# Performance work log

Hardware: AMD Instinct MI355X
Metric: run time of the kernel (lower is better)

## Reference

```python
import jax, jax.numpy as jnp
import numpy as np

N_EXPERTS = 8
TOP_K = 2
HIDDEN = 768
INTER = 2048

def setup_inputs() -> dict:
    key = jax.random.key(0)
    ks = jax.random.split(key, 12)
    s_in = 1.0 / np.sqrt(HIDDEN)
    s_mid = 1.0 / np.sqrt(INTER)
    return {
        "x": jax.random.normal(ks[0], (4, 64, 64, HIDDEN), dtype=jnp.float32),
        # gate: nn.Parameter(randn(E, d))
        "gate_w": jax.random.normal(ks[1], (N_EXPERTS, HIDDEN), dtype=jnp.float32),
        # routed experts, stacked: fc1 (d->f), fc2 (f->d)
        "fc1_w": jax.random.uniform(ks[2], (N_EXPERTS, INTER, HIDDEN), jnp.float32, -s_in, s_in),
        "fc1_b": jax.random.uniform(ks[3], (N_EXPERTS, INTER), jnp.float32, -s_in, s_in),
        "fc2_w": jax.random.uniform(ks[4], (N_EXPERTS, HIDDEN, INTER), jnp.float32, -s_mid, s_mid),
        "fc2_b": jax.random.uniform(ks[5], (N_EXPERTS, HIDDEN), jnp.float32, -s_mid, s_mid),
        # shared MLP (gated): w1 (d->f), w3 (d->f), w2 (f->d)
        "w1_w": jax.random.uniform(ks[6], (INTER, HIDDEN), jnp.float32, -s_in, s_in),
        "w1_b": jax.random.uniform(ks[7], (INTER,), jnp.float32, -s_in, s_in),
        "w3_w": jax.random.uniform(ks[8], (INTER, HIDDEN), jnp.float32, -s_in, s_in),
        "w3_b": jax.random.uniform(ks[9], (INTER,), jnp.float32, -s_in, s_in),
        "w2_w": jax.random.uniform(ks[10], (HIDDEN, INTER), jnp.float32, -s_mid, s_mid),
        "w2_b": jax.random.uniform(ks[11], (HIDDEN,), jnp.float32, -s_mid, s_mid),
    }

def _gelu(h):
    # torch nn.GELU / F.gelu default = exact (erf) form
    return jax.nn.gelu(h, approximate=False)

def reference(x, gate_w, fc1_w, fc1_b, fc2_w, fc2_b,
              w1_w, w1_b, w3_w, w3_b, w2_w, w2_b):
    B, H, W, C = x.shape
    xf = x.reshape(-1, C)                                  # [T, d]
    # gate: softmax over experts, top-k, renormalize
    scores = jax.nn.softmax(xf @ gate_w.T, axis=-1)        # [T, E]
    top_v, top_i = jax.lax.top_k(scores, TOP_K)            # [T, k]
    top_v = top_v / jnp.sum(top_v, axis=-1, keepdims=True)
    # routed experts: dense-mask combine (weight 0 => zero contribution,
    # same math as gather-GEMM-scatter without data-dependent shapes)
    out = jnp.zeros_like(xf)
    for e in range(N_EXPERTS):
        w_e = jnp.sum(jnp.where(top_i == e, top_v, 0.0), axis=-1)   # [T]
        h = _gelu(xf @ fc1_w[e].T + fc1_b[e])                        # [T, f]
        y = h @ fc2_w[e].T + fc2_b[e]                                # [T, d]
        out = out + w_e[:, None] * y
    # shared gated MLP
    shared = (_gelu(xf @ w1_w.T + w1_b) * (xf @ w3_w.T + w3_b)) @ w2_w.T + w2_b
    return (out + shared).reshape(B, H, W, C)
```

## Files before the change

### kernel.cpp

```cpp
#include <hip/hip_runtime.h>
#include <math.h>

#define T_TOK 16384
#define DH 768
#define DF 2048
#define NE 8
#define NSLOT (2 * T_TOK)
#define MT_ROUTED 264
#define NROW_H (MT_ROUTED * 128)

typedef __attribute__((ext_vector_type(8))) short bf16x8;
typedef __attribute__((ext_vector_type(4))) float f32x4;

__device__ __forceinline__ unsigned short f2bf(float f) {
  union { float f; unsigned int u; } v; v.f = f;
  unsigned int u = v.u;
  u += 0x7fffu + ((u >> 16) & 1u);
  return (unsigned short)(u >> 16);
}
__device__ __forceinline__ float bf2f(unsigned short s) {
  union { unsigned int u; float f; } v; v.u = ((unsigned int)s) << 16; return v.f;
}

__device__ __forceinline__ float gelu_exact(float x) {
  return 0.5f * x * (1.0f + erff(x * 0.70710678118654752440f));
}

__device__ __forceinline__ unsigned short* yrow(unsigned short* ylo,
                                                unsigned short* yhi, int s) {
  return (s < T_TOK) ? (ylo + (long)s * DH) : (yhi + (long)(s - T_TOK) * DH);
}

__device__ __forceinline__ void async_cp16(void* lds, const void* g) {
  __builtin_amdgcn_global_load_lds(
      (const __attribute__((address_space(1))) unsigned int*)(unsigned long long)g,
      (__attribute__((address_space(3))) unsigned int*)(unsigned int)(unsigned long long)lds,
      16, 0, 0);
}

__global__ __launch_bounds__(256) void conv_f32_bf16(
    const float* __restrict__ src, unsigned short* __restrict__ dst, int n4) {
  int i = blockIdx.x * blockDim.x + threadIdx.x;
  if (i >= n4) return;
  const float4 v = ((const float4*)src)[i];
  union { unsigned short us[4]; unsigned long long u64; } o;
  o.us[0] = f2bf(v.x); o.us[1] = f2bf(v.y); o.us[2] = f2bf(v.z); o.us[3] = f2bf(v.w);
  ((unsigned long long*)dst)[i] = o.u64;
}

__global__ __launch_bounds__(256) void gate_topk(
    const float* __restrict__ x, const float* __restrict__ gw,
    unsigned short* __restrict__ xb, int* __restrict__ eids,
    float* __restrict__ wts) {
  const int wave = threadIdx.x >> 6;
  const int lane = threadIdx.x & 63;
  const int t = blockIdx.x * 4 + wave;
  float4 xv[3];
#pragma unroll
  for (int i = 0; i < 3; ++i) {
    const int c = i * 256 + lane * 4;
    xv[i] = *(const float4*)&x[(long)t * DH + c];
    ushort4 o;
    o.x = f2bf(xv[i].x); o.y = f2bf(xv[i].y);
    o.z = f2bf(xv[i].z); o.w = f2bf(xv[i].w);
    *(ushort4*)&xb[(long)t * DH + c] = o;
  }
  float s[NE];
#pragma unroll
  for (int e = 0; e < NE; ++e) {
    float a = 0.f;
#pragma unroll
    for (int i = 0; i < 3; ++i) {
      const float4 g = *(const float4*)&gw[e * DH + i * 256 + lane * 4];
      a += xv[i].x * g.x + xv[i].y * g.y + xv[i].z * g.z + xv[i].w * g.w;
    }
    s[e] = a;
  }
#pragma unroll
  for (int off = 32; off >= 1; off >>= 1) {
#pragma unroll
    for (int e = 0; e < NE; ++e) s[e] += __shfl_xor(s[e], off);
  }
  if (lane == 0) {
    float b1 = s[0]; int i1 = 0;
#pragma unroll
    for (int e = 1; e < NE; ++e) { if (s[e] > b1) { b1 = s[e]; i1 = e; } }
    float b2 = -3.4e38f; int i2 = 0;
#pragma unroll
    for (int e = 0; e < NE; ++e) {
      if (e != i1 && s[e] > b2) { b2 = s[e]; i2 = e; }
    }
    const float ex = expf(b2 - b1);
    eids[2 * t]     = i1; wts[2 * t]     = 1.f / (1.f + ex);
    eids[2 * t + 1] = i2; wts[2 * t + 1] = ex / (1.f + ex);
  }
}

__global__ __launch_bounds__(256) void hist_k(
    const int* __restrict__ eids, int* __restrict__ hcur) {
  const int j = blockIdx.x * 256 + threadIdx.x;
  const int lane = threadIdx.x & 63;
  const int eid = eids[j];
#pragma unroll
  for (int e = 0; e < NE; ++e) {
    const unsigned long long m = __ballot(eid == e);
    const int tot = __popcll(m);
    if (tot && lane == (__ffsll((long long)m) - 1)) atomicAdd(&hcur[e * 64], tot);
  }
}

__global__ void scan_k(const int* __restrict__ hcur, int* __restrict__ sched,
                       int* __restrict__ cur2) {
  if (threadIdx.x == 0) {
    int b = 0;
#pragma unroll
    for (int e = 0; e < NE; ++e) {
      const int c = hcur[e * 64];
      sched[e] = b; sched[9 + e] = c; cur2[e * 64] = b;
      b += (c + 127) & ~127;
    }
    sched[8] = b;
  }
}

__global__ __launch_bounds__(256) void scatter_k(
    const int* __restrict__ eids, const float* __restrict__ wts,
    int* __restrict__ cur2, int* __restrict__ slot_tok,
    float* __restrict__ slot_wt, int* __restrict__ slot_pos) {
  const int j = blockIdx.x * 256 + threadIdx.x;
  const int lane = threadIdx.x & 63;
  const int eid = eids[j];
  const float w = wts[j];
#pragma unroll
  for (int e = 0; e < NE; ++e) {
    const unsigned long long m = __ballot(eid == e);
    const int tot = __popcll(m);
    if (!tot) continue;
    const int leader = __ffsll((long long)m) - 1;
    int b = 0;
    if (lane == leader) b = atomicAdd(&cur2[e * 64], tot);
    b = __shfl(b, leader);
    if (eid == e) {
      const int pos = b + __popcll(m & ((1ull << lane) - 1));
      slot_tok[pos] = j;
      slot_wt[pos] = w;
      slot_pos[j] = pos;
    }
  }
}

template <int MODE, int GX, int GTOT>
__global__ __launch_bounds__(256, 2) void gemm_k(
    const unsigned short* __restrict__ A, const unsigned short* __restrict__ B1,
    const unsigned short* __restrict__ B2, const float* __restrict__ bias1,
    const float* __restrict__ bias2, float* __restrict__ outF,
    unsigned short* __restrict__ outH, int K,
    const int* __restrict__ sched, const int* __restrict__ slot_tok,
    const int* __restrict__ slot_pos, const float* __restrict__ wts,
    unsigned short* __restrict__ ylo, unsigned short* __restrict__ yhi) {
  constexpr int BPX = (GTOT + 7) / 8;
  const int id = blockIdx.x;
  const int yx = (id & 7) * BPX + (id >> 3);
  const int n0 = (yx % GX) * 128;
  const int m0 = (yx / GX) * 128;

  const int tid = threadIdx.x;
  const int wave = tid >> 6;
  const int lane = tid & 63;
  const int wm = wave >> 1, wn = wave & 1;
  const int l16 = lane & 15, quad = lane >> 4;

  const unsigned short* Bbase = B1;
  const float* bias = bias1;
  int cnt_end = 0;
  if constexpr (MODE == 1 || MODE == 3 || MODE == 4) {
    if (m0 >= sched[8]) return;
    int e = 0;
#pragma unroll
    for (int i = 1; i < NE; ++i) { if (m0 >= sched[i]) e = i; }
    cnt_end = sched[e] + sched[9 + e];
    Bbase = B1 + (long)e * ((long)DF * DH);
    bias = bias1 + e * ((MODE == 1) ? DF : DH);
  }

  __shared__ __align__(16) unsigned short As[2][128 * 32];
  __shared__ __align__(16) unsigned short Bs[2][128 * 32];
  __shared__ __align__(16) unsigned short Cs[(MODE == 0) ? 2 : 1]
                                            [(MODE == 0) ? 128 * 32 : 16];

  const int srow0 = wave * 16 + (lane >> 2);
  const int srow1 = 64 + srow0;
  const int scol = (((lane & 3) ^ ((lane >> 3) & 3)) << 3);

  long ar0, ar1;
  if constexpr (MODE == 1) {
    const int p0 = m0 + srow0, p1 = m0 + srow1;
    const int t0 = (p0 < cnt_end) ? (slot_tok[p0] >> 1) : 0;
    const int t1 = (p1 < cnt_end) ? (slot_tok[p1] >> 1) : 0;
    ar0 = (long)t0 * K; ar1 = (long)t1 * K;
  } else {
    ar0 = (long)(m0 + srow0) * K;
    ar1 = (long)(m0 + srow1) * K;
  }
  const unsigned short* ap0 = A + ar0 + scol;
  const unsigned short* ap1 = A + ar1 + scol;
  const unsigned short* bp0 = Bbase + (long)(n0 + srow0) * K + scol;
  const unsigned short* bp1 = Bbase + (long)(n0 + srow1) * K + scol;
  const unsigned short* cp0 = nullptr; const unsigned short* cp1 = nullptr;
  if constexpr (MODE == 0) {
    cp0 = B2 + (long)(n0 + srow0) * K + scol;
    cp1 = B2 + (long)(n0 + srow1) * K + scol;
  }

  const int woff = wave * 512;

  f32x4 acc[4][4];
  f32x4 acc2[(MODE == 0) ? 4 : 1][(MODE == 0) ? 4 : 1];
#pragma unroll
  for (int i = 0; i < 4; ++i) {
#pragma unroll
    for (int j = 0; j < 4; ++j) {
      acc[i][j] = {0.f, 0.f, 0.f, 0.f};
      if constexpr (MODE == 0) acc2[i][j] = {0.f, 0.f, 0.f, 0.f};
    }
  }

  auto stage = [&](int b, int kt) {
    const int ko = kt << 5;
    async_cp16(&As[b][woff],        ap0 + ko);
    async_cp16(&As[b][woff + 2048], ap1 + ko);
    async_cp16(&Bs[b][woff],        bp0 + ko);
    async_cp16(&Bs[b][woff + 2048], bp1 + ko);
    if constexpr (MODE == 0) {
      async_cp16(&Cs[b][woff],        cp0 + ko);
      async_cp16(&Cs[b][woff + 2048], cp1 + ko);
    }
  };

  const int rchunk = ((quad ^ ((l16 >> 1) & 3)) << 3);

  const int KT = K >> 5;
  stage(0, 0);
  __syncthreads();

  for (int kt = 0; kt < KT; ++kt) {
    const int b = kt & 1;
    if (kt + 1 < KT) stage(b ^ 1, kt + 1);

    bf16x8 af[4], bfr[4], cfr[(MODE == 0) ? 4 : 1];
#pragma unroll
    for (int mi = 0; mi < 4; ++mi)
      af[mi] = *(const bf16x8*)&As[b][(wm * 64 + mi * 16 + l16) * 32 + rchunk];
#pragma unroll
    for (int ni = 0; ni < 4; ++ni) {
      bfr[ni] = *(const bf16x8*)&Bs[b][(wn * 64 + ni * 16 + l16) * 32 + rchunk];
      if constexpr (MODE == 0)
        cfr[ni] = *(const bf16x8*)&Cs[b][(wn * 64 + ni * 16 + l16) * 32 + rchunk];
    }
#pragma unroll
    for (int mi = 0; mi < 4; ++mi) {
#pragma unroll
      for (int ni = 0; ni < 4; ++ni) {
        acc[mi][ni] = __builtin_amdgcn_mfma_f32_16x16x32_bf16(
            af[mi], bfr[ni], acc[mi][ni], 0, 0, 0);
        if constexpr (MODE == 0)
          acc2[mi][ni] = __builtin_amdgcn_mfma_f32_16x16x32_bf16(
              af[mi], cfr[ni], acc2[mi][ni], 0, 0, 0);
      }
    }
    __syncthreads();
  }

#pragma unroll
  for (int mi = 0; mi < 4; ++mi) {
#pragma unroll
    for (int r = 0; r < 4; ++r) {
      const int row = m0 + wm * 64 + mi * 16 + quad * 4 + r;
      if constexpr (MODE == 3) {
        unsigned short* yr = yrow(ylo, yhi, row);
#pragma unroll
        for (int ni = 0; ni < 4; ++ni) {
          const int c = n0 + wn * 64 + ni * 16 + l16;
          yr[c] = f2bf(acc[mi][ni][r] + bias[c]);
        }
      } else if constexpr (MODE == 4) {
        if (row < cnt_end) {
          const int t = slot_tok[row] >> 1;
          const float w = wts[row];
#pragma unroll
          for (int ni = 0; ni < 4; ++ni) {
            const int c = n0 + wn * 64 + ni * 16 + l16;
            atomicAdd(&outF[(long)t * DH + c], w * (acc[mi][ni][r] + bias[c]));
          }
        }
      } else if constexpr (MODE == 2) {
        const int s0 = slot_pos[2 * row], s1 = slot_pos[2 * row + 1];
        const float w0 = wts[2 * row], w1 = wts[2 * row + 1];
        const unsigned short* y0 = yrow(ylo, yhi, s0);
        const unsigned short* y1 = yrow(ylo, yhi, s1);
#pragma unroll
        for (int ni = 0; ni < 4; ++ni) {
          const int c = n0 + wn * 64 + ni * 16 + l16;
          outF[(long)row * DH + c] =
              acc[mi][ni][r] + bias[c] + w0 * bf2f(y0[c]) + w1 * bf2f(y1[c]);
        }
      } else if constexpr (MODE == 5) {
#pragma unroll
        for (int ni = 0; ni < 4; ++ni) {
          const int c = n0 + wn * 64 + ni * 16 + l16;
          outF[(long)row * DH + c] = acc[mi][ni][r] + bias[c];
        }
      } else if constexpr (MODE == 1) {
#pragma unroll
        for (int ni = 0; ni < 4; ++ni) {
          const int c = n0 + wn * 64 + ni * 16 + l16;
          outH[(long)row * DF + c] = f2bf(gelu_exact(acc[mi][ni][r] + bias[c]));
        }
      } else {
#pragma unroll
        for (int ni = 0; ni < 4; ++ni) {
          const int c = n0 + wn * 64 + ni * 16 + l16;
          const float h1 = acc[mi][ni][r] + bias[c];
          const float h3 = acc2[mi][ni][r] + bias2[c];
          outH[(long)row * DF + c] = f2bf(gelu_exact(h1) * h3);
        }
      }
    }
  }
}

extern "C" void kernel_launch(void* const* d_in, const int* in_sizes, int n_in,
                              void* d_out, int out_size, void* d_ws, size_t ws_size,
                              hipStream_t stream) {
  const float* x     = (const float*)d_in[0];
  const float* gw    = (const float*)d_in[1];
  const float* fc1w  = (const float*)d_in[2];
  const float* fc1bs = (const float*)d_in[3];
  const float* fc2w  = (const float*)d_in[4];
  const float* fc2bs = (const float*)d_in[5];
  const float* w1w   = (const float*)d_in[6];
  const float* w1bs  = (const float*)d_in[7];
  const float* w3w   = (const float*)d_in[8];
  const float* w3bs  = (const float*)d_in[9];
  const float* w2w   = (const float*)d_in[10];
  const float* w2bs  = (const float*)d_in[11];
  float* out = (float*)d_out;

  char* p = (char*)d_ws;
  auto take = [&](size_t b) { char* r = p; p += (b + 255) & ~(size_t)255; return r; };
  unsigned short* xb   = (unsigned short*)take((size_t)T_TOK * DH * 2);
  unsigned short* fc1b = (unsigned short*)take((size_t)NE * DF * DH * 2);
  unsigned short* fc2b = (unsigned short*)take((size_t)NE * DH * DF * 2);
  unsigned short* w1b  = (unsigned short*)take((size_t)DF * DH * 2);
  unsigned short* w3b  = (unsigned short*)take((size_t)DF * DH * 2);
  unsigned short* w2b  = (unsigned short*)take((size_t)DH * DF * 2);
  unsigned short* h    = (unsigned short*)take((size_t)NROW_H * DF * 2);
  int*   eids     = (int*)take((size_t)NSLOT * 4);
  float* wts      = (float*)take((size_t)NSLOT * 4);
  int*   hcur     = (int*)take(NE * 64 * 4);
  int*   cur2     = (int*)take(NE * 64 * 4);
  int*   sched    = (int*)take(32 * 4);
  int*   slot_tok = (int*)take((size_t)NROW_H * 4);
  float* slot_wt  = (float*)take((size_t)NROW_H * 4);
  int*   slot_pos = (int*)take((size_t)NSLOT * 4);

  const size_t yhi_bytes = (size_t)(NROW_H - T_TOK) * DH * 2;
  const bool pathA = ((size_t)(p - (char*)d_ws) + yhi_bytes) <= ws_size;
  unsigned short* ylo = fc1b;
  unsigned short* yhi = pathA ? (unsigned short*)take(yhi_bytes) : nullptr;

  hipMemsetAsync(hcur, 0, NE * 64 * sizeof(int), stream);

  auto conv = [&](const float* s, unsigned short* d, long n) {
    int n4 = (int)(n >> 2);
    conv_f32_bf16<<<(n4 + 255) / 256, 256, 0, stream>>>(s, d, n4);
  };
  conv(fc1w, fc1b, (long)NE * DF * DH);
  conv(fc2w, fc2b, (long)NE * DH * DF);
  conv(w1w, w1b, (long)DF * DH);
  conv(w3w, w3b, (long)DF * DH);
  conv(w2w, w2b, (long)DH * DF);

  gate_topk<<<T_TOK / 4, 256, 0, stream>>>(x, gw, xb, eids, wts);
  hist_k<<<NSLOT / 256, 256, 0, stream>>>(eids, hcur);
  scan_k<<<1, 64, 0, stream>>>(hcur, sched, cur2);
  scatter_k<<<NSLOT / 256, 256, 0, stream>>>(eids, wts, cur2, slot_tok, slot_wt,
                                             slot_pos);

  if (pathA) {
    gemm_k<1, 16, 16 * MT_ROUTED><<<16 * MT_ROUTED, 256, 0, stream>>>(
        xb, fc1b, nullptr, fc1bs, nullptr, nullptr, h, DH,
        sched, slot_tok, nullptr, nullptr, nullptr, nullptr);
    gemm_k<3, 6, 6 * MT_ROUTED><<<6 * MT_ROUTED, 256, 0, stream>>>(
        h, fc2b, nullptr, fc2bs, nullptr, nullptr, nullptr, DF,
        sched, nullptr, nullptr, nullptr, ylo, yhi);
    gemm_k<0, 16, 16 * (T_TOK / 128)><<<16 * (T_TOK / 128), 256, 0, stream>>>(
        xb, w1b, w3b, w1bs, w3bs, nullptr, h, DH,
        nullptr, nullptr, nullptr, nullptr, nullptr, nullptr);
    gemm_k<2, 6, 6 * (T_TOK / 128)><<<6 * (T_TOK / 128), 256, 0, stream>>>(
        h, w2b, nullptr, w2bs, nullptr, out, nullptr, DF,
        nullptr, nullptr, slot_pos, wts, ylo, yhi);
  } else {
    gemm_k<0, 16, 16 * (T_TOK / 128)><<<16 * (T_TOK / 128), 256, 0, stream>>>(
        xb, w1b, w3b, w1bs, w3bs, nullptr, h, DH,
        nullptr, nullptr, nullptr, nullptr, nullptr, nullptr);
    gemm_k<5, 6, 6 * (T_TOK / 128)><<<6 * (T_TOK / 128), 256, 0, stream>>>(
        h, w2b, nullptr, w2bs, nullptr, out, nullptr, DF,
        nullptr, nullptr, nullptr, nullptr, nullptr, nullptr);
    gemm_k<1, 16, 16 * MT_ROUTED><<<16 * MT_ROUTED, 256, 0, stream>>>(
        xb, fc1b, nullptr, fc1bs, nullptr, nullptr, h, DH,
        sched, slot_tok, nullptr, nullptr, nullptr, nullptr);
    gemm_k<4, 6, 6 * MT_ROUTED><<<6 * MT_ROUTED, 256, 0, stream>>>(
        h, fc2b, nullptr, fc2bs, nullptr, out, nullptr, DF,
        sched, slot_tok, nullptr, slot_wt, nullptr, nullptr);
  }
}
```

Measured before the change: 734.9 us.

## Interleave w1/w3 rows into one weight matrix and use fast erf GELU

Converts w1 and w3 into a single bf16 matrix whose rows alternate in groups of 16, so the shared gated GEMM becomes a plain single-B GEMM with N=4096. Each tile's accumulators hold paired w1/w3 columns that are combined in the epilogue, which removes the second LDS buffer, the second accumulator set and its register pressure. Separately, erff is replaced by an Abramowitz-Stegun polynomial built on a hardware reciprocal and exp2, which lowers epilogue cost at a small accuracy loss (about 1e-7 absolute on erf). The grid for the shared fc1 stage doubles, with each block covering half as many output channels.

```diff
diff --git a/kernel.cpp b/kernel.cpp
--- a/kernel.cpp
+++ b/kernel.cpp
@@ -22,8 +22,30 @@
   union { unsigned int u; float f; } v; v.u = ((unsigned int)s) << 16; return v.f;
 }
 
-__device__ __forceinline__ float gelu_exact(float x) {
-  return 0.5f * x * (1.0f + erff(x * 0.70710678118654752440f));
+#if __has_builtin(__builtin_amdgcn_rcpf)
+#define RCPF(x) __builtin_amdgcn_rcpf(x)
+#else
+#define RCPF(x) (1.0f / (x))
+#endif
+#if __has_builtin(__builtin_amdgcn_exp2f)
+#define EXP2F(x) __builtin_amdgcn_exp2f(x)
+#else
+#define EXP2F(x) exp2f(x)
+#endif
+
+__device__ __forceinline__ float gelu_fast(float x) {
+  const float z = 0.70710678118654752440f * x;
+  const float a = fabsf(z);
+  const float t = RCPF(fmaf(0.3275911f, a, 1.0f));
+  float p = fmaf(1.061405429f, t, -1.453152027f);
+  p = fmaf(p, t, 1.421413741f);
+  p = fmaf(p, t, -0.284496736f);
+  p = fmaf(p, t, 0.254829592f);
+  p = p * t;
+  const float e = EXP2F(z * z * -1.4426950408889634f);
+  const float erfa = fmaf(-p, e, 1.0f);
+  const float erfz = copysignf(erfa, z);
+  return 0.5f * x * (1.0f + erfz);
 }
 
 __device__ __forceinline__ unsigned short* yrow(unsigned short* ylo,
@@ -46,6 +68,20 @@
   union { unsigned short us[4]; unsigned long long u64; } o;
   o.us[0] = f2bf(v.x); o.us[1] = f2bf(v.y); o.us[2] = f2bf(v.z); o.us[3] = f2bf(v.w);
   ((unsigned long long*)dst)[i] = o.u64;
+}
+
+__global__ __launch_bounds__(192) void conv_interleave_k(
+    const float* __restrict__ w1, const float* __restrict__ w3,
+    unsigned short* __restrict__ dst) {
+  const int row = blockIdx.x;
+  const int q = row >> 5, s = row & 31;
+  const float* src = (s < 16) ? &w1[(long)(q * 16 + s) * DH]
+                              : &w3[(long)(q * 16 + (s - 16)) * DH];
+  const int c = threadIdx.x * 4;
+  const float4 v = *(const float4*)&src[c];
+  ushort4 o;
+  o.x = f2bf(v.x); o.y = f2bf(v.y); o.z = f2bf(v.z); o.w = f2bf(v.w);
+  *(ushort4*)&dst[(long)row * DH + c] = o;
 }
 
 __global__ __launch_bounds__(256) void gate_topk(
@@ -152,9 +188,8 @@
 template <int MODE, int GX, int GTOT>
 __global__ __launch_bounds__(256, 2) void gemm_k(
     const unsigned short* __restrict__ A, const unsigned short* __restrict__ B1,
-    const unsigned short* __restrict__ B2, const float* __restrict__ bias1,
-    const float* __restrict__ bias2, float* __restrict__ outF,
-    unsigned short* __restrict__ outH, int K,
+    const float* __restrict__ bias1, const float* __restrict__ bias2,
+    float* __restrict__ outF, unsigned short* __restrict__ outH, int K,
     const int* __restrict__ sched, const int* __restrict__ slot_tok,
     const int* __restrict__ slot_pos, const float* __restrict__ wts,
     unsigned short* __restrict__ ylo, unsigned short* __restrict__ yhi) {
@@ -185,8 +220,6 @@
 
   __shared__ __align__(16) unsigned short As[2][128 * 32];
   __shared__ __align__(16) unsigned short Bs[2][128 * 32];
-  __shared__ __align__(16) unsigned short Cs[(MODE == 0) ? 2 : 1]
-                                            [(MODE == 0) ? 128 * 32 : 16];
 
   const int srow0 = wave * 16 + (lane >> 2);
   const int srow1 = 64 + srow0;
@@ -206,24 +239,14 @@
   const unsigned short* ap1 = A + ar1 + scol;
   const unsigned short* bp0 = Bbase + (long)(n0 + srow0) * K + scol;
   const unsigned short* bp1 = Bbase + (long)(n0 + srow1) * K + scol;
-  const unsigned short* cp0 = nullptr; const unsigned short* cp1 = nullptr;
-  if constexpr (MODE == 0) {
-    cp0 = B2 + (long)(n0 + srow0) * K + scol;
-    cp1 = B2 + (long)(n0 + srow1) * K + scol;
-  }
 
   const int woff = wave * 512;
 
   f32x4 acc[4][4];
-  f32x4 acc2[(MODE == 0) ? 4 : 1][(MODE == 0) ? 4 : 1];
-#pragma unroll
-  for (int i = 0; i < 4; ++i) {
-#pragma unroll
-    for (int j = 0; j < 4; ++j) {
-      acc[i][j] = {0.f, 0.f, 0.f, 0.f};
-      if constexpr (MODE == 0) acc2[i][j] = {0.f, 0.f, 0.f, 0.f};
-    }
-  }
+#pragma unroll
+  for (int i = 0; i < 4; ++i)
+#pragma unroll
+    for (int j = 0; j < 4; ++j) acc[i][j] = {0.f, 0.f, 0.f, 0.f};
 
   auto stage = [&](int b, int kt) {
     const int ko = kt << 5;
@@ -231,10 +254,6 @@
     async_cp16(&As[b][woff + 2048], ap1 + ko);
     async_cp16(&Bs[b][woff],        bp0 + ko);
     async_cp16(&Bs[b][woff + 2048], bp1 + ko);
-    if constexpr (MODE == 0) {
-      async_cp16(&Cs[b][woff],        cp0 + ko);
-      async_cp16(&Cs[b][woff + 2048], cp1 + ko);
-    }
   };
 
   const int rchunk = ((quad ^ ((l16 >> 1) & 3)) << 3);
@@ -247,25 +266,19 @@
     const int b = kt & 1;
     if (kt + 1 < KT) stage(b ^ 1, kt + 1);
 
-    bf16x8 af[4], bfr[4], cfr[(MODE == 0) ? 4 : 1];
+    bf16x8 af[4], bfr[4];
 #pragma unroll
     for (int mi = 0; mi < 4; ++mi)
       af[mi] = *(const bf16x8*)&As[b][(wm * 64 + mi * 16 + l16) * 32 + rchunk];
 #pragma unroll
-    for (int ni = 0; ni < 4; ++ni) {
+    for (int ni = 0; ni < 4; ++ni)
       bfr[ni] = *(const bf16x8*)&Bs[b][(wn * 64 + ni * 16 + l16) * 32 + rchunk];
-      if constexpr (MODE == 0)
-        cfr[ni] = *(const bf16x8*)&Cs[b][(wn * 64 + ni * 16 + l16) * 32 + rchunk];
-    }
 #pragma unroll
     for (int mi = 0; mi < 4; ++mi) {
 #pragma unroll
       for (int ni = 0; ni < 4; ++ni) {
         acc[mi][ni] = __builtin_amdgcn_mfma_f32_16x16x32_bf16(
             af[mi], bfr[ni], acc[mi][ni], 0, 0, 0);
-        if constexpr (MODE == 0)
-          acc2[mi][ni] = __builtin_amdgcn_mfma_f32_16x16x32_bf16(
-              af[mi], cfr[ni], acc2[mi][ni], 0, 0, 0);
       }
     }
     __syncthreads();
@@ -314,15 +327,15 @@
 #pragma unroll
         for (int ni = 0; ni < 4; ++ni) {
           const int c = n0 + wn * 64 + ni * 16 + l16;
-          outH[(long)row * DF + c] = f2bf(gelu_exact(acc[mi][ni][r] + bias[c]));
+          outH[(long)row * DF + c] = f2bf(gelu_fast(acc[mi][ni][r] + bias[c]));
         }
       } else {
 #pragma unroll
-        for (int ni = 0; ni < 4; ++ni) {
-          const int c = n0 + wn * 64 + ni * 16 + l16;
-          const float h1 = acc[mi][ni][r] + bias[c];
-          const float h3 = acc2[mi][ni][r] + bias2[c];
-          outH[(long)row * DF + c] = f2bf(gelu_exact(h1) * h3);
+        for (int p = 0; p < 2; ++p) {
+          const int ch = ((n0 + wn * 64) >> 1) + p * 16 + l16;
+          const float h1 = acc[mi][2 * p][r] + bias1[ch];
+          const float h3 = acc[mi][2 * p + 1][r] + bias2[ch];
+          outH[(long)row * DF + ch] = f2bf(gelu_fast(h1) * h3);
         }
       }
     }
@@ -351,8 +364,7 @@
   unsigned short* xb   = (unsigned short*)take((size_t)T_TOK * DH * 2);
   unsigned short* fc1b = (unsigned short*)take((size_t)NE * DF * DH * 2);
   unsigned short* fc2b = (unsigned short*)take((size_t)NE * DH * DF * 2);
-  unsigned short* w1b  = (unsigned short*)take((size_t)DF * DH * 2);
-  unsigned short* w3b  = (unsigned short*)take((size_t)DF * DH * 2);
+  unsigned short* bint = (unsigned short*)take((size_t)2 * DF * DH * 2);
   unsigned short* w2b  = (unsigned short*)take((size_t)DH * DF * 2);
   unsigned short* h    = (unsigned short*)take((size_t)NROW_H * DF * 2);
   int*   eids     = (int*)take((size_t)NSLOT * 4);
@@ -377,9 +389,8 @@
   };
   conv(fc1w, fc1b, (long)NE * DF * DH);
   conv(fc2w, fc2b, (long)NE * DH * DF);
-  conv(w1w, w1b, (long)DF * DH);
-  conv(w3w, w3b, (long)DF * DH);
   conv(w2w, w2b, (long)DH * DF);
+  conv_interleave_k<<<2 * DF, 192, 0, stream>>>(w1w, w3w, bint);
 
   gate_topk<<<T_TOK / 4, 256, 0, stream>>>(x, gw, xb, eids, wts);
   hist_k<<<NSLOT / 256, 256, 0, stream>>>(eids, hcur);
@@ -389,29 +400,29 @@
 
   if (pathA) {
     gemm_k<1, 16, 16 * MT_ROUTED><<<16 * MT_ROUTED, 256, 0, stream>>>(
-        xb, fc1b, nullptr, fc1bs, nullptr, nullptr, h, DH,
+        xb, fc1b, fc1bs, nullptr, nullptr, h, DH,
         sched, slot_tok, nullptr, nullptr, nullptr, nullptr);
     gemm_k<3, 6, 6 * MT_ROUTED><<<6 * MT_ROUTED, 256, 0, stream>>>(
-        h, fc2b, nullptr, fc2bs, nullptr, nullptr, nullptr, DF,
+        h, fc2b, fc2bs, nullptr, nullptr, nullptr, DF,
         sched, nullptr, nullptr, nullptr, ylo, yhi);
-    gemm_k<0, 16, 16 * (T_TOK / 128)><<<16 * (T_TOK / 128), 256, 0, stream>>>(
-        xb, w1b, w3b, w1bs, w3bs, nullptr, h, DH,
+    gemm_k<0, 32, 32 * (T_TOK / 128)><<<32 * (T_TOK / 128), 256, 0, stream>>>(
+        xb, bint, w1bs, w3bs, nullptr, h, DH,
         nullptr, nullptr, nullptr, nullptr, nullptr, nullptr);
     gemm_k<2, 6, 6 * (T_TOK / 128)><<<6 * (T_TOK / 128), 256, 0, stream>>>(
-        h, w2b, nullptr, w2bs, nullptr, out, nullptr, DF,
+        h, w2b, w2bs, nullptr, out, nullptr, DF,
         nullptr, nullptr, slot_pos, wts, ylo, yhi);
   } else {
-    gemm_k<0, 16, 16 * (T_TOK / 128)><<<16 * (T_TOK / 128), 256, 0, stream>>>(
-        xb, w1b, w3b, w1bs, w3bs, nullptr, h, DH,
+    gemm_k<0, 32, 32 * (T_TOK / 128)><<<32 * (T_TOK / 128), 256, 0, stream>>>(
+        xb, bint, w1bs, w3bs, nullptr, h, DH,
         nullptr, nullptr, nullptr, nullptr, nullptr, nullptr);
     gemm_k<5, 6, 6 * (T_TOK / 128)><<<6 * (T_TOK / 128), 256, 0, stream>>>(
-        h, w2b, nullptr, w2bs, nullptr, out, nullptr, DF,
+        h, w2b, w2bs, nullptr, out, nullptr, DF,
         nullptr, nullptr, nullptr, nullptr, nullptr, nullptr);
     gemm_k<1, 16, 16 * MT_ROUTED><<<16 * MT_ROUTED, 256, 0, stream>>>(
-        xb, fc1b, nullptr, fc1bs, nullptr, nullptr, h, DH,
+        xb, fc1b, fc1bs, nullptr, nullptr, h, DH,
         sched, slot_tok, nullptr, nullptr, nullptr, nullptr);
     gemm_k<4, 6, 6 * MT_ROUTED><<<6 * MT_ROUTED, 256, 0, stream>>>(
-        h, fc2b, nullptr, fc2bs, nullptr, out, nullptr, DF,
+        h, fc2b, fc2bs, nullptr, out, nullptr, DF,
         sched, slot_tok, nullptr, slot_wt, nullptr, nullptr);
   }
 }
```

Result: no change. 722.0 us (-1.8%).
